# Kernel tuning notes

Hardware: AMD Instinct MI355X
Metric: run time of the kernel (lower is better)

## Reference

```python
import jax, jax.numpy as jnp
import numpy as np
import math

MAXL = 2
N = 256
TAU = 8


def _cg_coeff(j1, m1, j2, m2, J, M):
    if m1 + m2 != M or J < abs(j1 - j2) or J > j1 + j2:
        return 0.0
    f = math.factorial
    pre = math.sqrt((2 * J + 1) * f(J + j1 - j2) * f(J - j1 + j2) * f(j1 + j2 - J) / f(j1 + j2 + J + 1))
    pre *= math.sqrt(f(J + M) * f(J - M) * f(j1 - m1) * f(j1 + m1) * f(j2 - m2) * f(j2 + m2))
    kmin = max(0, j2 - J - m1, j1 + m2 - J)
    kmax = min(j1 + j2 - J, j1 - m1, j2 + m2)
    s = 0.0
    for k in range(kmin, kmax + 1):
        s += (-1.0) ** k / (f(k) * f(j1 + j2 - J - k) * f(j1 - m1 - k) * f(j2 + m2 - k) * f(J - j2 + m1 + k) * f(J - j1 - m2 + k))
    return pre * s


def _cg_tensor(l1, l2, L):
    C = np.zeros((2 * l1 + 1, 2 * l2 + 1, 2 * L + 1), np.float32)
    for m1 in range(-l1, l1 + 1):
        for m2 in range(-l2, l2 + 1):
            M = m1 + m2
            if -L <= M <= L:
                C[m1 + l1, m2 + l2, M + L] = _cg_coeff(l1, m1, l2, m2, L, M)
    return C

_CG = {}
for _l1 in range(MAXL + 1):
    for _l2 in range(MAXL + 1):
        for _L in range(abs(_l1 - _l2), min(_l1 + _l2, MAXL) + 1):
            _CG[(_l1, _l2, _L)] = _cg_tensor(_l1, _l2, _L)


def _cgproduct(xs, ys, maxl):
    # xs[l]: [..., 2l+1, tau_x], ys[l]: [..., 2l+1, tau_y]
    out = []
    for L in range(maxl + 1):
        chunks = []
        for l1 in range(maxl + 1):
            for l2 in range(maxl + 1):
                if abs(l1 - l2) <= L <= l1 + l2:
                    C = jnp.asarray(_CG[(l1, l2, L)])
                    t = jnp.einsum('...mc,...nd,mnM->...Mcd', xs[l1], ys[l2], C)
                    sh = t.shape
                    chunks.append(t.reshape(sh[:-2] + (sh[-2] * sh[-1],)))
        out.append(jnp.concatenate(chunks, axis=-1))
    return out


def _forward(v0, v1, v2, adj, s0, s1, s2, wn0, wn1, wn2, wr0, wr1, wr2):
    v = [v0, v1, v2]                       # [N, 1, 2l+1, tau]
    sph = [s0[None], s1[None], s2[None]]   # [1, N, N, 2l+1, 1]
    wn = [wn0, wn1, wn2]
    wr = [wr0, wr1, wr2]
    # message pass: gather/sum over neighbors (Rmask1 gather)
    vmp = [jnp.einsum('ij,jamc->iamc', adj, p)[None] for p in v]  # [1, N, 1, 2l+1, tau]
    # first CG product (vertex x vertex)
    cg_nl = _cgproduct(vmp, vmp, MAXL)
    # per-l channel mixing with weights_nl
    mixed = [jnp.einsum('bxymc,cd->bxymd', cg_nl[l], wn[l]) for l in range(MAXL + 1)]
    # repeat to pairwise adims [N, N] (broadcast over second array dim)
    n = adj.shape[0]
    rep = [jnp.broadcast_to(m, (1, n, n, m.shape[3], m.shape[4])) for m in mixed]
    # second CG product with relative-position spherical harmonics
    cg_rel = _cgproduct(rep, sph, MAXL)
    # per-cell mixing with weights_rel
    mixed_rel = [jnp.einsum('bxymc,xycd->bxymd', cg_rel[l], wr[l]) for l in range(MAXL + 1)]
    # sum over source-node array dim
    vsum = [jnp.sum(m, axis=1) for m in mixed_rel]  # [1, N, 2l+1, tau]
    # NormalizeVecArr mutates parts in place -> returned vertices_sum is normalized
    out = [p / jnp.sum(p) for p in vsum]
    # concatenate parts along m-axis for a single output array [1, N, 9, tau]
    return jnp.concatenate(out, axis=2)


def setup_inputs() -> dict:
    key = jax.random.key(0)
    ks = jax.random.split(key, 13)
    d = {}
    d['v0'] = jax.random.normal(ks[0], (N, 1, 1, TAU), jnp.float32)
    d['v1'] = jax.random.normal(ks[1], (N, 1, 3, TAU), jnp.float32)
    d['v2'] = jax.random.normal(ks[2], (N, 1, 5, TAU), jnp.float32)
    d['adj'] = jax.random.uniform(ks[3], (N, N), jnp.float32)
    d['s0'] = jax.random.normal(ks[4], (N, N, 1, 1), jnp.float32)
    d['s1'] = jax.random.normal(ks[5], (N, N, 3, 1), jnp.float32)
    d['s2'] = jax.random.normal(ks[6], (N, N, 5, 1), jnp.float32)
    W = 0.05
    d['wn0'] = W * jax.random.normal(ks[7], (192, TAU), jnp.float32)
    d['wn1'] = W * jax.random.normal(ks[8], (384, TAU), jnp.float32)
    d['wn2'] = W * jax.random.normal(ks[9], (384, TAU), jnp.float32)
    d['wr0'] = W * jax.random.normal(ks[10], (N, N, 24, TAU), jnp.float32)
    d['wr1'] = W * jax.random.normal(ks[11], (N, N, 48, TAU), jnp.float32)
    d['wr2'] = W * jax.random.normal(ks[12], (N, N, 48, TAU), jnp.float32)
    return d


def reference(v0, v1, v2, adj, s0, s1, s2, wn0, wn1, wn2, wr0, wr1, wr2):
    return _forward(v0, v1, v2, adj, s0, s1, s2, wn0, wn1, wn2, wr0, wr1, wr2)
```

## Files before the change

kernel.cpp:

```cpp
#include <hip/hip_runtime.h>

#define NN 256
#define XPW 8
#define NXS (NN/(4*XPW))

#define C13  0.5773502691896258f
#define C15  0.4472135954999579f
#define CC12 0.7071067811865476f
#define S35  0.7745966692414834f
#define S310 0.5477225575051661f
#define C110 0.3162277660168379f
#define S25  0.6324555320336759f
#define S23  0.8164965809277260f
#define C16  0.4082482904638630f
#define S27  0.5345224838248488f
#define S37  0.6546536707079771f
#define C114 0.2672612419124244f

#define CGREL(mx, sv, r0, r1, r2) \
    r0[0] = mx[0]*sv[0]; \
    r0[1] = C13*(mx[1]*sv[3] - mx[2]*sv[2] + mx[3]*sv[1]); \
    r0[2] = C15*(mx[4]*sv[8] - mx[5]*sv[7] + mx[6]*sv[6] - mx[7]*sv[5] + mx[8]*sv[4]); \
    r1[0][0] = mx[0]*sv[1]; r1[1][0] = mx[0]*sv[2]; r1[2][0] = mx[0]*sv[3]; \
    r1[0][1] = mx[1]*sv[0]; r1[1][1] = mx[2]*sv[0]; r1[2][1] = mx[3]*sv[0]; \
    r1[0][2] = CC12*(mx[2]*sv[1] - mx[1]*sv[2]); \
    r1[1][2] = CC12*(mx[3]*sv[1] - mx[1]*sv[3]); \
    r1[2][2] = CC12*(mx[3]*sv[2] - mx[2]*sv[3]); \
    r1[0][3] = S35*mx[3]*sv[4] - S310*mx[2]*sv[5] + C110*mx[1]*sv[6]; \
    r1[1][3] = S310*(mx[3]*sv[5] + mx[1]*sv[7]) - S25*mx[2]*sv[6]; \
    r1[2][3] = S35*mx[1]*sv[8] - S310*mx[2]*sv[7] + C110*mx[3]*sv[6]; \
    r1[0][4] = C110*mx[6]*sv[1] - S310*mx[5]*sv[2] + S35*mx[4]*sv[3]; \
    r1[1][4] = S310*(mx[7]*sv[1] + mx[5]*sv[3]) - S25*mx[6]*sv[2]; \
    r1[2][4] = S35*mx[8]*sv[1] - S310*mx[7]*sv[2] + C110*mx[6]*sv[3]; \
    r1[0][5] = C15*(mx[7]*sv[4] - mx[4]*sv[7]) + S310*(mx[5]*sv[6] - mx[6]*sv[5]); \
    r1[1][5] = S25*(mx[8]*sv[4] - mx[4]*sv[8]) + C110*(mx[5]*sv[7] - mx[7]*sv[5]); \
    r1[2][5] = C15*(mx[8]*sv[5] - mx[5]*sv[8]) + S310*(mx[6]*sv[7] - mx[7]*sv[6]); \
    r2[0][0]=mx[0]*sv[4]; r2[1][0]=mx[0]*sv[5]; r2[2][0]=mx[0]*sv[6]; r2[3][0]=mx[0]*sv[7]; r2[4][0]=mx[0]*sv[8]; \
    r2[0][1] = mx[1]*sv[1]; \
    r2[1][1] = CC12*(mx[2]*sv[1] + mx[1]*sv[2]); \
    r2[2][1] = C16*(mx[3]*sv[1] + mx[1]*sv[3]) + S23*mx[2]*sv[2]; \
    r2[3][1] = CC12*(mx[3]*sv[2] + mx[2]*sv[3]); \
    r2[4][1] = mx[3]*sv[3]; \
    r2[0][2] = S23*mx[2]*sv[4] - C13*mx[1]*sv[5]; \
    r2[1][2] = C13*mx[3]*sv[4] + C16*mx[2]*sv[5] - CC12*mx[1]*sv[6]; \
    r2[2][2] = CC12*(mx[3]*sv[5] - mx[1]*sv[7]); \
    r2[3][2] = CC12*mx[3]*sv[6] - C16*mx[2]*sv[7] - C13*mx[1]*sv[8]; \
    r2[4][2] = C13*mx[3]*sv[7] - S23*mx[2]*sv[8]; \
    r2[0][3]=mx[4]*sv[0]; r2[1][3]=mx[5]*sv[0]; r2[2][3]=mx[6]*sv[0]; r2[3][3]=mx[7]*sv[0]; r2[4][3]=mx[8]*sv[0]; \
    r2[0][4] = C13*mx[5]*sv[1] - S23*mx[4]*sv[2]; \
    r2[1][4] = CC12*mx[6]*sv[1] - C16*mx[5]*sv[2] - C13*mx[4]*sv[3]; \
    r2[2][4] = CC12*(mx[7]*sv[1] - mx[5]*sv[3]); \
    r2[3][4] = C13*mx[8]*sv[1] + C16*mx[7]*sv[2] - CC12*mx[6]*sv[3]; \
    r2[4][4] = S23*mx[8]*sv[2] - C13*mx[7]*sv[3]; \
    r2[0][5] = S27*(mx[4]*sv[6] + mx[6]*sv[4]) - S37*mx[5]*sv[5]; \
    r2[1][5] = S37*(mx[4]*sv[7] + mx[7]*sv[4]) - C114*(mx[5]*sv[6] + mx[6]*sv[5]); \
    r2[2][5] = S27*(mx[8]*sv[4] + mx[4]*sv[8] - mx[6]*sv[6]) + C114*(mx[7]*sv[5] + mx[5]*sv[7]); \
    r2[3][5] = S37*(mx[8]*sv[5] + mx[5]*sv[8]) - C114*(mx[7]*sv[6] + mx[6]*sv[7]); \
    r2[4][5] = S27*(mx[8]*sv[6] + mx[6]*sv[8]) - S37*mx[7]*sv[7];

__global__ __launch_bounds__(256) void k_nodes(
                        const float* __restrict__ adj,
                        const float* __restrict__ v0,
                        const float* __restrict__ v1,
                        const float* __restrict__ v2,
                        const float* __restrict__ wn0,
                        const float* __restrict__ wn1,
                        const float* __restrict__ wn2,
                        float* __restrict__ mixed,
                        float* __restrict__ psum){
  __shared__ float part[4][72];
  int i = blockIdx.x;
  int tid = threadIdx.x, wv = tid >> 6, lane = tid & 63;
  if (i == 0 && tid < 3) psum[tid] = 0.f;
  {
    const float* vp1; int st1;
    if (lane < 8)       { vp1 = v0 + lane;      st1 = 8;  }
    else if (lane < 32) { vp1 = v1 + (lane-8);  st1 = 24; }
    else                { vp1 = v2 + (lane-32); st1 = 40; }
    const float* vp2 = v2 + 32 + lane;
    const float* arow = adj + i*NN;
    int j0 = wv*64;
    float a1a = 0.f, a1b = 0.f, a2a = 0.f, a2b = 0.f;
    #pragma unroll 8
    for (int j = j0; j < j0+64; j += 2){
      float av0 = arow[j], av1 = arow[j+1];
      a1a = fmaf(av0, vp1[j*st1], a1a);
      a1b = fmaf(av1, vp1[(j+1)*st1], a1b);
      if (lane < 8){
        a2a = fmaf(av0, vp2[j*40], a2a);
        a2b = fmaf(av1, vp2[(j+1)*40], a2b);
      }
    }
    part[wv][lane] = a1a + a1b;
    if (lane < 8) part[wv][64+lane] = a2a + a2b;
  }
  __syncthreads();
  if (wv) return;
  {
    float s = part[0][lane] + part[1][lane] + part[2][lane] + part[3][lane];
    float s2 = 0.f;
    if (lane < 8)
      s2 = part[0][64+lane] + part[1][64+lane] + part[2][64+lane] + part[3][64+lane];
    part[0][lane] = s;
    if (lane < 8) part[0][64+lane] = s2;
  }
  int c = lane >> 3, d = lane & 7;
  float mx[9], sv[9];
  #pragma unroll
  for (int j=0;j<9;j++){ mx[j] = part[0][j*8 + c]; sv[j] = part[0][j*8 + d]; }
  float r0[3], r1[3][6], r2[5][6];
  CGREL(mx, sv, r0, r1, r2)

  float a0[8], a1m[3][8], a2m[5][8];
  #pragma unroll
  for (int dp=0;dp<8;dp++){ a0[dp]=0.f;
    #pragma unroll
    for (int M=0;M<3;M++) a1m[M][dp]=0.f;
    #pragma unroll
    for (int M=0;M<5;M++) a2m[M][dp]=0.f;
  }
  #pragma unroll
  for (int k=0;k<3;k++){
    const float* row = wn0 + (k*64 + lane)*8;
    float4 u = *(const float4*)row;
    float4 v = *(const float4*)(row+4);
    float u8[8] = {u.x,u.y,u.z,u.w,v.x,v.y,v.z,v.w};
    #pragma unroll
    for (int dp=0;dp<8;dp++) a0[dp] = fmaf(r0[k], u8[dp], a0[dp]);
  }
  #pragma unroll
  for (int k=0;k<6;k++){
    const float* row = wn1 + (k*64 + lane)*8;
    float4 u = *(const float4*)row;
    float4 v = *(const float4*)(row+4);
    float u8[8] = {u.x,u.y,u.z,u.w,v.x,v.y,v.z,v.w};
    #pragma unroll
    for (int M=0;M<3;M++)
      #pragma unroll
      for (int dp=0;dp<8;dp++) a1m[M][dp] = fmaf(r1[M][k], u8[dp], a1m[M][dp]);
  }
  #pragma unroll
  for (int k=0;k<6;k++){
    const float* row = wn2 + (k*64 + lane)*8;
    float4 u = *(const float4*)row;
    float4 v = *(const float4*)(row+4);
    float u8[8] = {u.x,u.y,u.z,u.w,v.x,v.y,v.z,v.w};
    #pragma unroll
    for (int M=0;M<5;M++)
      #pragma unroll
      for (int dp=0;dp<8;dp++) a2m[M][dp] = fmaf(r2[M][k], u8[dp], a2m[M][dp]);
  }
  #pragma unroll
  for (int m=0;m<9;m++){
    #pragma unroll
    for (int dp=0;dp<8;dp++){
      float val = (m==0) ? a0[dp] : (m<4 ? a1m[m-1][dp] : a2m[m-4][dp]);
      val += __shfl_xor(val, 1);
      val += __shfl_xor(val, 2);
      val += __shfl_xor(val, 4);
      val += __shfl_xor(val, 8);
      val += __shfl_xor(val, 16);
      val += __shfl_xor(val, 32);
      if (lane == ((m*8+dp) & 63)) mixed[i*72 + m*8 + dp] = val;
    }
  }
}

__global__ __launch_bounds__(256) void k_pair(
    const float* __restrict__ mixed,
    const float* __restrict__ s0, const float* __restrict__ s1, const float* __restrict__ s2,
    const float* __restrict__ wr0, const float* __restrict__ wr1, const float* __restrict__ wr2,
    float* __restrict__ part, float* __restrict__ psum){
  __shared__ float red[4][72];
  __shared__ float bp[3];
  int tid = threadIdx.x;
  int wv = tid >> 6, lane = tid & 63;
  int y = blockIdx.x & (NN-1);
  int xsel = blockIdx.x >> 8;
  int xbase = (xsel*4 + wv) * XPW;
  int cgp = lane >> 3;

  float acc[9];
  #pragma unroll
  for (int m=0;m<9;m++) acc[m]=0.f;

  for (int i=0;i<XPW;i++){
    int x = xbase + i;
    int pxy = x*NN + y;
    const float* p0 = wr0 + (size_t)pxy*192 + lane;
    const float* p1 = wr1 + (size_t)pxy*384 + lane;
    const float* p2 = wr2 + (size_t)pxy*384 + lane;
    float w0v[3], w1v[6], w2v[6];
    #pragma unroll
    for (int k=0;k<3;k++) w0v[k] = __builtin_nontemporal_load(p0 + k*64);
    #pragma unroll
    for (int k=0;k<6;k++) w1v[k] = __builtin_nontemporal_load(p1 + k*64);
    #pragma unroll
    for (int k=0;k<6;k++) w2v[k] = __builtin_nontemporal_load(p2 + k*64);

    float mx[9], sv[9];
    {
      const float* mb = mixed + x*72 + cgp;
      #pragma unroll
      for (int j=0;j<9;j++) mx[j] = mb[j*8];
      sv[0] = s0[pxy];
      #pragma unroll
      for (int j=0;j<3;j++) sv[1+j] = s1[(size_t)pxy*3+j];
      #pragma unroll
      for (int j=0;j<5;j++) sv[4+j] = s2[(size_t)pxy*5+j];
    }

    float r0[3], r1[3][6], r2[5][6];
    CGREL(mx, sv, r0, r1, r2)

    #pragma unroll
    for (int k=0;k<3;k++) acc[0] = fmaf(r0[k], w0v[k], acc[0]);
    #pragma unroll
    for (int k=0;k<6;k++){
      acc[1] = fmaf(r1[0][k], w1v[k], acc[1]);
      acc[2] = fmaf(r1[1][k], w1v[k], acc[2]);
      acc[3] = fmaf(r1[2][k], w1v[k], acc[3]);
      acc[4] = fmaf(r2[0][k], w2v[k], acc[4]);
      acc[5] = fmaf(r2[1][k], w2v[k], acc[5]);
      acc[6] = fmaf(r2[2][k], w2v[k], acc[6]);
      acc[7] = fmaf(r2[3][k], w2v[k], acc[7]);
      acc[8] = fmaf(r2[4][k], w2v[k], acc[8]);
    }
  }

  #pragma unroll
  for (int m=0;m<9;m++){
    float v = acc[m];
    v += __shfl_xor(v, 8);
    v += __shfl_xor(v, 16);
    v += __shfl_xor(v, 32);
    acc[m] = v;
  }
  if (lane < 8){
    #pragma unroll
    for (int m=0;m<9;m++) red[wv][m*8+lane] = acc[m];
  }
  if (tid < 3) bp[tid] = 0.f;
  __syncthreads();
  if (tid < 72){
    float v = red[0][tid] + red[1][tid] + red[2][tid] + red[3][tid];
    part[((size_t)xsel*NN + y)*72 + tid] = v;
    int mall = tid >> 3;
    int l = (mall==0) ? 0 : (mall < 4 ? 1 : 2);
    atomicAdd(&bp[l], v);
  }
  __syncthreads();
  if (tid < 3) atomicAdd(&psum[tid], bp[tid]);
}

__global__ __launch_bounds__(256) void k_final(
    const float* __restrict__ part, const float* __restrict__ psum,
    float* __restrict__ out){
  int idx = blockIdx.x*256 + threadIdx.x;
  int y = idx / 72;
  int t = idx - y*72;
  float v = 0.f;
  #pragma unroll
  for (int x=0; x<NXS; x++) v += part[((size_t)x*NN + y)*72 + t];
  int mall = t >> 3;
  float den = (mall == 0) ? psum[0] : (mall < 4 ? psum[1] : psum[2]);
  out[idx] = v / den;
}

extern "C" void kernel_launch(void* const* d_in, const int* in_sizes, int n_in,
                              void* d_out, int out_size, void* d_ws, size_t ws_size,
                              hipStream_t stream) {
  const float* v0  = (const float*)d_in[0];
  const float* v1  = (const float*)d_in[1];
  const float* v2  = (const float*)d_in[2];
  const float* adj = (const float*)d_in[3];
  const float* s0  = (const float*)d_in[4];
  const float* s1  = (const float*)d_in[5];
  const float* s2  = (const float*)d_in[6];
  const float* wn0 = (const float*)d_in[7];
  const float* wn1 = (const float*)d_in[8];
  const float* wn2 = (const float*)d_in[9];
  const float* wr0 = (const float*)d_in[10];
  const float* wr1 = (const float*)d_in[11];
  const float* wr2 = (const float*)d_in[12];
  float* out = (float*)d_out;

  float* ws    = (float*)d_ws;
  float* mixed = ws;
  float* part  = ws + 18432;
  float* psum  = ws + 18432 + 147456;

  k_nodes<<<NN, 256, 0, stream>>>(adj, v0, v1, v2, wn0, wn1, wn2, mixed, psum);
  k_pair<<<NN*NXS, 256, 0, stream>>>(mixed, s0, s1, s2, wr0, wr1, wr2, part, psum);
  k_final<<<72, 256, 0, stream>>>(part, psum, out);
}
```

Measured before the change: 79.73 us.

## Vectorize wr loads as float4 and remap lanes to channel pairs

Each lane in k_pair now reads the rotation-weight tensors with 16-byte float4 nontemporal loads instead of strided scalar loads. Lanes are remapped so a pair of lanes covers one CG channel and the two halves of the 8 output taus. The CG-product terms are chosen per lane with select logic, and partial sums are kept in vf4 accumulators. This cuts the number of load instructions on the dominant memory stream. In exchange it adds select ALU work, idle lanes for the smaller weight tensors, and more shuffle reduction steps (36 values over 5 levels instead of 9 over 3).

```diff
diff --git a/kernel.cpp b/kernel.cpp
--- a/kernel.cpp
+++ b/kernel.cpp
@@ -3,6 +3,8 @@
 #define NN 256
 #define XPW 8
 #define NXS (NN/(4*XPW))
+
+typedef float vf4 __attribute__((ext_vector_type(4)));
 
 #define C13  0.5773502691896258f
 #define C15  0.4472135954999579f
@@ -166,6 +168,16 @@
   }
 }
 
+__device__ __forceinline__ float sel3(float a0, float a1, float a2, int k){
+  float r = (k==1) ? a1 : a0;
+  return (k>=2) ? a2 : r;
+}
+__device__ __forceinline__ float sel4(float a0, float a1, float a2, float a3, int k){
+  float lo = (k&1) ? a1 : a0;
+  float hi = (k&1) ? a3 : a2;
+  return (k&2) ? hi : lo;
+}
+
 __global__ __launch_bounds__(256) void k_pair(
     const float* __restrict__ mixed,
     const float* __restrict__ s0, const float* __restrict__ s1, const float* __restrict__ s2,
@@ -178,29 +190,35 @@
   int y = blockIdx.x & (NN-1);
   int xsel = blockIdx.x >> 8;
   int xbase = (xsel*4 + wv) * XPW;
-  int cgp = lane >> 3;
-
-  float acc[9];
-  #pragma unroll
-  for (int m=0;m<9;m++) acc[m]=0.f;
+
+  int c2 = lane >> 1, dq = lane & 1;
+  int tc = c2 & 7;
+  int c0c = (c2 < 24) ? c2 : 23;
+  int cb  = c2 & 15;
+  int k0  = c2 >> 3;
+  int kb  = cb >> 3;
+  bool v0ok = (c2 < 24);
+  bool vbok = (c2 < 16);
+
+  vf4 acc[9];
+  #pragma unroll
+  for (int m=0;m<9;m++) acc[m] = (vf4)0.f;
 
   for (int i=0;i<XPW;i++){
     int x = xbase + i;
     int pxy = x*NN + y;
-    const float* p0 = wr0 + (size_t)pxy*192 + lane;
-    const float* p1 = wr1 + (size_t)pxy*384 + lane;
-    const float* p2 = wr2 + (size_t)pxy*384 + lane;
-    float w0v[3], w1v[6], w2v[6];
-    #pragma unroll
-    for (int k=0;k<3;k++) w0v[k] = __builtin_nontemporal_load(p0 + k*64);
-    #pragma unroll
-    for (int k=0;k<6;k++) w1v[k] = __builtin_nontemporal_load(p1 + k*64);
-    #pragma unroll
-    for (int k=0;k<6;k++) w2v[k] = __builtin_nontemporal_load(p2 + k*64);
+    const vf4* q0 = (const vf4*)(wr0 + (size_t)pxy*192);
+    const vf4* q1 = (const vf4*)(wr1 + (size_t)pxy*384);
+    const vf4* q2 = (const vf4*)(wr2 + (size_t)pxy*384);
+    vf4 w0  = __builtin_nontemporal_load(q0 + (c0c*2 + dq));
+    vf4 w1a = __builtin_nontemporal_load(q1 + (c2*2 + dq));
+    vf4 w1b = __builtin_nontemporal_load(q1 + ((32+cb)*2 + dq));
+    vf4 w2a = __builtin_nontemporal_load(q2 + (c2*2 + dq));
+    vf4 w2b = __builtin_nontemporal_load(q2 + ((32+cb)*2 + dq));
 
     float mx[9], sv[9];
     {
-      const float* mb = mixed + x*72 + cgp;
+      const float* mb = mixed + x*72 + tc;
       #pragma unroll
       for (int j=0;j<9;j++) mx[j] = mb[j*8];
       sv[0] = s0[pxy];
@@ -213,32 +231,43 @@
     float r0[3], r1[3][6], r2[5][6];
     CGREL(mx, sv, r0, r1, r2)
 
-    #pragma unroll
-    for (int k=0;k<3;k++) acc[0] = fmaf(r0[k], w0v[k], acc[0]);
-    #pragma unroll
-    for (int k=0;k<6;k++){
-      acc[1] = fmaf(r1[0][k], w1v[k], acc[1]);
-      acc[2] = fmaf(r1[1][k], w1v[k], acc[2]);
-      acc[3] = fmaf(r1[2][k], w1v[k], acc[3]);
-      acc[4] = fmaf(r2[0][k], w2v[k], acc[4]);
-      acc[5] = fmaf(r2[1][k], w2v[k], acc[5]);
-      acc[6] = fmaf(r2[2][k], w2v[k], acc[6]);
-      acc[7] = fmaf(r2[3][k], w2v[k], acc[7]);
-      acc[8] = fmaf(r2[4][k], w2v[k], acc[8]);
-    }
+    float g0 = v0ok ? sel3(r0[0], r0[1], r0[2], k0) : 0.f;
+    float g1a[3], g1b[3], g2a[5], g2b[5];
+    #pragma unroll
+    for (int M=0;M<3;M++){
+      g1a[M] = sel4(r1[M][0], r1[M][1], r1[M][2], r1[M][3], k0);
+      g1b[M] = vbok ? (kb ? r1[M][5] : r1[M][4]) : 0.f;
+    }
+    #pragma unroll
+    for (int M=0;M<5;M++){
+      g2a[M] = sel4(r2[M][0], r2[M][1], r2[M][2], r2[M][3], k0);
+      g2b[M] = vbok ? (kb ? r2[M][5] : r2[M][4]) : 0.f;
+    }
+
+    acc[0] += g0 * w0;
+    #pragma unroll
+    for (int M=0;M<3;M++) acc[1+M] += g1a[M]*w1a + g1b[M]*w1b;
+    #pragma unroll
+    for (int M=0;M<5;M++) acc[4+M] += g2a[M]*w2a + g2b[M]*w2b;
   }
 
   #pragma unroll
   for (int m=0;m<9;m++){
-    float v = acc[m];
-    v += __shfl_xor(v, 8);
-    v += __shfl_xor(v, 16);
-    v += __shfl_xor(v, 32);
-    acc[m] = v;
-  }
-  if (lane < 8){
-    #pragma unroll
-    for (int m=0;m<9;m++) red[wv][m*8+lane] = acc[m];
+    #pragma unroll
+    for (int comp=0;comp<4;comp++){
+      float v = acc[m][comp];
+      v += __shfl_xor(v, 2);
+      v += __shfl_xor(v, 4);
+      v += __shfl_xor(v, 8);
+      v += __shfl_xor(v, 16);
+      v += __shfl_xor(v, 32);
+      acc[m][comp] = v;
+    }
+  }
+  if (lane < 2){
+    #pragma unroll
+    for (int m=0;m<9;m++)
+      *(vf4*)&red[wv][m*8 + lane*4] = acc[m];
   }
   if (tid < 3) bp[tid] = 0.f;
   __syncthreads();
```

Result: slower. 87.11 us (+9.3%).
